# Kernel optimization log

Hardware: AMD Instinct MI355X
Metric: run time of the kernel (lower is better)

Reference implementation:

```python
import math
import jax, jax.numpy as jnp
import numpy as np

B_IN, B_OUT = 16, 16
F_IN, F_OUT, BATCH = 32, 64, 4
N_ALPHA, N_GAMMA = 4, 3
KERNEL_BETA = math.pi / 8.0
L_TOT = sum((2 * l + 1) ** 2 for l in range(B_OUT))  # 5456


def _lg(n):
    return math.lgamma(n + 1.0)


def _small_d(l, beta):
    """Wigner small-d matrix d^l_{m,n}(beta), [2l+1, 2l+1], Condon-Shortley phase."""
    c, s = math.cos(0.5 * beta), math.sin(0.5 * beta)
    d = np.zeros((2 * l + 1, 2 * l + 1), dtype=np.float64)
    for mi, m in enumerate(range(-l, l + 1)):
        for ni, n in enumerate(range(-l, l + 1)):
            pref = 0.5 * (_lg(l + m) + _lg(l - m) + _lg(l + n) + _lg(l - n))
            acc = 0.0
            for k in range(max(0, n - m), min(l + n, l - m) + 1):
                ln = pref - _lg(l + n - k) - _lg(k) - _lg(m - n + k) - _lg(l - m - k)
                acc += ((-1.0) ** (m - n + k)) * math.exp(ln) * (c ** (2 * l + n - m - 2 * k)) * (s ** (m - n + 2 * k))
            d[mi, ni] = acc
    return d


def _qweights(b):
    """Kostelec-Rockmore SOFT quadrature weights over the 2b beta samples."""
    k = np.arange(b)
    w = np.array([
        (2.0 / b) * math.sin(math.pi * (2 * j + 1) / (4.0 * b)) *
        np.sum(np.sin((2 * j + 1) * (2 * k + 1) * math.pi / (4.0 * b)) / (2 * k + 1))
        for j in range(2 * b)])
    return w


def _wigner_table(betas, b_out, scale_fn):
    rows = []
    for beta in betas:
        blocks = [(_small_d(l, beta) * scale_fn(l)).ravel() for l in range(b_out)]
        rows.append(np.concatenate(blocks))
    return np.stack(rows)  # [len(betas), L_TOT]


def _grid_basis(grid, b_out):
    """conj(D^l_{mn}(a,b,g)) = e^{+i m a} d^l_{mn}(b) e^{+i n g}, flattened over (l,m,n)."""
    cols = []
    for (a, bb, g) in grid:
        blocks = []
        for l in range(b_out):
            m = np.arange(-l, l + 1)
            d = _small_d(l, bb)
            ph = np.exp(1j * (m[:, None] * a + m[None, :] * g))
            blocks.append((d * ph).ravel())
        cols.append(np.concatenate(blocks))
    return np.stack(cols, axis=1)  # [L_TOT, n_grid] complex


def _freq_indices(b_out, nfft):
    ms, ns = [], []
    for l in range(b_out):
        r = np.arange(-l, l + 1)
        M, N = np.meshgrid(r, r, indexing='ij')
        ms.append(np.mod(M.ravel(), nfft))
        ns.append(np.mod(N.ravel(), nfft))
    return np.concatenate(ms), np.concatenate(ns)


def make_grid():
    alphas = [2.0 * math.pi * i / N_ALPHA for i in range(N_ALPHA)]
    gammas = [2.0 * math.pi * i / N_GAMMA for i in range(N_GAMMA)]
    return [(a, KERNEL_BETA, g) for a in alphas for g in gammas]


def setup_inputs() -> dict:
    key = jax.random.key(0)
    k1, k2 = jax.random.split(key)
    x = jax.random.normal(k1, (BATCH, F_IN, 2 * B_IN, 2 * B_IN, 2 * B_IN), jnp.float32)
    grid = make_grid()
    n_grid = len(grid)
    stdv = 1.0 / math.sqrt(n_grid * F_IN * (B_OUT ** 3) / float(B_IN ** 3))
    kernel = stdv * jax.random.normal(k2, (F_IN, F_OUT, n_grid), jnp.float32)
    bias = jnp.zeros((1, F_OUT, 1, 1, 1), jnp.float32)
    # analysis table: quadrature weight * d, with (2pi/2b)^2/(8pi^2) = 1/(8 b^2) absorbed
    betas_in = np.pi * (2 * np.arange(2 * B_IN) + 1) / (4.0 * B_IN)
    w = _qweights(B_IN) / (8.0 * B_IN ** 2)
    wig_f = _wigner_table(betas_in, B_OUT, lambda l: 1.0) * w[:, None]
    # synthesis table: (2l+1) * d, times (2b)^2 to cancel ifft2 normalization
    betas_out = np.pi * (2 * np.arange(2 * B_OUT) + 1) / (4.0 * B_OUT)
    wig_i = _wigner_table(betas_out, B_OUT, lambda l: (2 * l + 1) * (2 * B_OUT) ** 2)
    D = _grid_basis(grid, B_OUT)
    return {
        'x': x, 'kernel': kernel, 'bias': bias,
        'wigner_fwd': jnp.asarray(wig_f, jnp.float32),
        'wigner_inv': jnp.asarray(wig_i, jnp.float32),
        'D_re': jnp.asarray(D.real, jnp.float32),
        'D_im': jnp.asarray(D.imag, jnp.float32),
    }


def reference(x, kernel, bias, wigner_fwd, wigner_inv, D_re, D_im):
    batch, fin = x.shape[0], x.shape[1]
    fout = kernel.shape[1]
    midx_in, nidx_in = _freq_indices(B_OUT, 2 * B_IN)
    midx_out, nidx_out = _freq_indices(B_OUT, 2 * B_OUT)
    # --- SO3 FFT of input: FFT over (alpha, gamma), weighted beta-sum with Wigner-d ---
    Xf = jnp.fft.fft2(x.astype(jnp.complex64), axes=(-2, -1))   # [z,i,beta,ma,ng]
    Xg = Xf[..., midx_in, nidx_in]                               # [z,i,beta,L]
    xh = jnp.einsum('bl,zibl->lzi', wigner_fwd.astype(jnp.complex64), Xg)  # [L,z,i]
    # --- local FT of kernel on SO(3) grid points ---
    Dc = jax.lax.complex(D_re, D_im)                             # [L, n_grid]
    yh = jnp.einsum('lj,ioj->lio', Dc, kernel.astype(jnp.complex64))       # [L,i,o]
    # --- per-frequency block matmul (SO3_mm): z^l = x^l @ y^l, contracting f_in ---
    zs, begin = [], 0
    for l in range(B_OUT):
        n = 2 * l + 1
        xl = xh[begin:begin + n * n].reshape(n, n, batch, fin)
        yl = yh[begin:begin + n * n].reshape(n, n, fin, fout)
        zs.append(jnp.einsum('mkzi,knio->mnzo', xl, yl).reshape(n * n, batch, fout))
        begin += n * n
    zh = jnp.concatenate(zs, axis=0)                             # [L,z,o]
    # --- inverse SO3 FFT: scatter (l,m,n) -> FFT bins, ifft over (alpha,gamma) ---
    term = jnp.einsum('bl,lzo->zobl', wigner_inv.astype(jnp.complex64), zh)
    ng = 2 * B_OUT
    Zf = jnp.zeros((batch, fout, ng, ng, ng), jnp.complex64)
    Zf = Zf.at[..., midx_out, nidx_out].add(term)
    out = jnp.fft.ifft2(Zf, axes=(-2, -1)).real.astype(x.dtype)
    return out + bias
```

## Files before the change

### kernel.cpp

```cpp
#include <hip/hip_runtime.h>
#include <math.h>


typedef unsigned short u16;
typedef unsigned int   u32;
typedef __attribute__((ext_vector_type(8))) short  short8;
typedef __attribute__((ext_vector_type(4))) float  floatx4;

constexpr int LTOT = 5456;

constexpr int LB[17] = {0,1,10,35,84,165,286,455,680,969,
                        1330,1771,2300,2925,3654,4495,5456};

__device__ inline u16 f2bf(float f) {
    u32 u = __float_as_uint(f);
    u += 0x7fff + ((u >> 16) & 1);
    return (u16)(u >> 16);
}
__device__ inline u32 pack2bf(float re, float im) {
    return (u32)f2bf(re) | ((u32)f2bf(im) << 16);
}

__global__ __launch_bounds__(256) void k_wtr(const float* __restrict__ w,
                                             float* __restrict__ wT) {
    int t  = blockIdx.x * 256 + threadIdx.x;
    int bq = blockIdx.y;
    if (t < LTOT) {
        float4 v;
        v.x = w[(size_t)(bq * 4 + 0) * LTOT + t];
        v.y = w[(size_t)(bq * 4 + 1) * LTOT + t];
        v.z = w[(size_t)(bq * 4 + 2) * LTOT + t];
        v.w = w[(size_t)(bq * 4 + 3) * LTOT + t];
        *(float4*)(wT + ((size_t)bq * LTOT + t) * 4) = v;
    }
}

__global__ __launch_bounds__(512) void k_fft_fwd(const float* __restrict__ x,
                                                 u32* __restrict__ Xfb) {
    __shared__ float xs[1056];
    __shared__ float Gre[1056], Gim[1056];
    __shared__ float Wc[32], Ws[32];
    int tid = threadIdx.x;
    if (tid < 32) {
        float sv, cv;
        sincosf(6.28318530717958647692f * (float)tid / 32.0f, &sv, &cv);
        Wc[tid] = cv; Ws[tid] = sv;
    }
    const float* src = x + (size_t)blockIdx.x * 1024;
    for (int e = tid; e < 1024; e += 512) xs[(e >> 5) * 33 + (e & 31)] = src[e];
    __syncthreads();
    {
        int a = tid >> 4, k = tid & 15;
        const float* row = &xs[a * 33];
        float Er = 0.f, Ei = 0.f, Or = 0.f, Oi = 0.f;
#pragma unroll
        for (int h = 0; h < 16; h++) {
            int idx = (2 * h * k) & 31;
            float c = Wc[idx], s = Ws[idx];
            float xe = row[2 * h], xo = row[2 * h + 1];
            Er += xe * c;  Ei -= xe * s;
            Or += xo * c;  Oi -= xo * s;
        }
        float WOr = Or * Wc[k] + Oi * Ws[k];
        float WOi = Oi * Wc[k] - Or * Ws[k];
        Gre[a * 33 + k]      = Er + WOr;
        Gim[a * 33 + k]      = Ei + WOi;
        Gre[a * 33 + k + 16] = Er - WOr;
        Gim[a * 33 + k + 16] = Ei - WOi;
    }
    __syncthreads();
    {
        u32* dst = Xfb + (size_t)blockIdx.x * 512;
        int ng = tid & 31, ma = tid >> 5;
        float Er = 0.f, Ei = 0.f, Or = 0.f, Oi = 0.f;
#pragma unroll
        for (int h = 0; h < 16; h++) {
            int idx = (2 * h * ma) & 31;
            float c = Wc[idx], s = Ws[idx];
            float er = Gre[(2 * h) * 33 + ng],      ei = Gim[(2 * h) * 33 + ng];
            float orr = Gre[(2 * h + 1) * 33 + ng], oi = Gim[(2 * h + 1) * 33 + ng];
            Er += er * c + ei * s;   Ei += ei * c - er * s;
            Or += orr * c + oi * s;  Oi += oi * c - orr * s;
        }
        float WOr = Or * Wc[ma] + Oi * Ws[ma];
        float WOi = Oi * Wc[ma] - Or * Ws[ma];
        dst[ma * 32 + ng] = pack2bf(Er + WOr, Ei + WOi);
    }
}

__global__ __launch_bounds__(256) void k_prep_B(const float* __restrict__ Dre,
                                                const float* __restrict__ Dim,
                                                const float* __restrict__ ker,
                                                u32* __restrict__ yhb) {
    __shared__ float Ds[8][24];
    int t0  = blockIdx.x * 8;
    int tid = threadIdx.x;
    if (tid < 192) {
        int rr = tid / 24, jj = tid - rr * 24;
        Ds[rr][jj] = (jj < 12) ? Dre[(t0 + rr) * 12 + jj] : Dim[(t0 + rr) * 12 + jj - 12];
    }
    __syncthreads();
    for (int rep = 0; rep < 8; rep++) {
        int io = rep * 256 + tid;
        const float4* kp = (const float4*)(ker + io * 12);
        float4 ka = kp[0], kb = kp[1], kc = kp[2];
        float kv[12] = {ka.x, ka.y, ka.z, ka.w, kb.x, kb.y, kb.z, kb.w,
                        kc.x, kc.y, kc.z, kc.w};
#pragma unroll
        for (int rr = 0; rr < 8; rr++) {
            float sr = 0.f, si = 0.f;
#pragma unroll
            for (int j = 0; j < 12; j++) {
                sr += Ds[rr][j]      * kv[j];
                si += Ds[rr][12 + j] * kv[j];
            }
            yhb[(size_t)(t0 + rr) * 2048 + io] = pack2bf(sr, si);
        }
    }
}

__global__ __launch_bounds__(256) void k_beta_A(const u32* __restrict__ Xfb,
                                                const float* __restrict__ wfT,
                                                u16* __restrict__ Ab) {
    int ma  = blockIdx.x >> 6;
    int zig = blockIdx.x & 63;
    int tid = threadIdx.x;
    int ng  = tid & 31;
    int lq  = (tid >> 5) & 3;
    int zil = tid >> 7;
    int zi  = zig * 2 + zil;
    int z = zi >> 5, i = zi & 31;
    int mh = (ma <= 15) ? ma : ma - 32;
    int nh = (ng <= 15) ? ng : ng - 32;
    int am = mh < 0 ? -mh : mh;
    int an = nh < 0 ? -nh : nh;
    int l0 = am > an ? am : an;
    int lb = lq * 4;

    int isconj = (ma > 16);
    int mau = isconj ? (32 - ma) : ma;
    int ngu = isconj ? ((32 - ng) & 31) : ng;
    if (mau > 15) { mau = 0; ngu = 0; }

    int tl[4];
#pragma unroll
    for (int j = 0; j < 4; j++) {
        int l = lb + j;
        tl[j] = LB[l] + (mh + l) * (2 * l + 1) + (nh + l);
    }
    float2 acc[4];
#pragma unroll
    for (int j = 0; j < 4; j++) acc[j] = make_float2(0.f, 0.f);

    const u32* xp = Xfb + (size_t)zi * 32 * 512 + mau * 32 + ngu;
    float sgn = isconj ? -1.f : 1.f;
#pragma unroll 2
    for (int bq = 0; bq < 8; bq++) {
        u32 p0 = xp[(size_t)(4 * bq + 0) * 512];
        u32 p1 = xp[(size_t)(4 * bq + 1) * 512];
        u32 p2 = xp[(size_t)(4 * bq + 2) * 512];
        u32 p3 = xp[(size_t)(4 * bq + 3) * 512];
        float vx0 = __uint_as_float(p0 << 16);
        float vy0 = sgn * __uint_as_float(p0 & 0xffff0000u);
        float vx1 = __uint_as_float(p1 << 16);
        float vy1 = sgn * __uint_as_float(p1 & 0xffff0000u);
        float vx2 = __uint_as_float(p2 << 16);
        float vy2 = sgn * __uint_as_float(p2 & 0xffff0000u);
        float vx3 = __uint_as_float(p3 << 16);
        float vy3 = sgn * __uint_as_float(p3 & 0xffff0000u);
        const float4* wq = (const float4*)(wfT + (size_t)bq * (LTOT * 4));
#pragma unroll
        for (int j = 0; j < 4; j++) {
            if (lb + j >= l0) {
                float4 w = wq[tl[j]];
                acc[j].x += w.x * vx0 + w.y * vx1 + w.z * vx2 + w.w * vx3;
                acc[j].y += w.x * vy0 + w.y * vy1 + w.z * vy2 + w.w * vy3;
            }
        }
    }
    int s_i  = i >> 4;
    int kl   = 2 * (i & 15);
    int joff = kl & 7;
    int Lhi  = (kl >> 3) << 4;
#pragma unroll
    for (int j = 0; j < 4; j++) {
        int l = lb + j;
        if (l >= l0) {
            int mi = mh + l, ni = nh + l;
            int s   = 2 * ni + s_i;
            int row = 4 * mi + z;
            u32 pack = pack2bf(acc[j].x, acc[j].y);
            size_t off = (size_t)8192 * l * l + (size_t)s * 4096
                       + ((row >> 4) << 9) + ((Lhi + (row & 15)) << 3) + joff;
            *(u32*)(Ab + off) = pack;
        }
    }
}

__global__ __launch_bounds__(256) void k_gemm(const u16* __restrict__ Ab,
                                              const u32* __restrict__ yhb,
                                              float* __restrict__ zhT) {
    __shared__ __align__(16) u16 As[4096];
    __shared__ __align__(16) u16 Bs[2048];

    int rem = blockIdx.x, l, nl = 1;
    for (l = 15; l >= 0; l--) {
        nl = 2 * l + 1;
        int c = nl * 2;
        if (rem < c) break;
        rem -= c;
    }
    int n  = rem >> 1;
    int oh = rem & 1;
    int base = LB[l];
    const u16* Ag = Ab + (size_t)8192 * l * l;
    int S = 2 * nl;

    int tid = threadIdx.x, lane = tid & 63, w = tid >> 6;

    int kh = (tid >> 4) & 3;
    int nu = ((tid >> 6) << 4) + (tid & 15);
    int oo = (oh << 5) + (nu >> 1);
    int cc = nu & 1;

    floatx4 acc[2][4];
#pragma unroll
    for (int a = 0; a < 2; a++)
#pragma unroll
        for (int b = 0; b < 4; b++) acc[a][b] = (floatx4)0.f;

    for (int s = 0; s < S; s++) {
        const uint4* ap = (const uint4*)(Ag + (size_t)s * 4096);
        uint4 a0 = ap[tid * 2], a1 = ap[tid * 2 + 1];
        int k = s >> 1, ih = s & 1;
        const u32* yr = yhb + (size_t)(base + k * nl + n) * 2048
                        + (((ih << 4) + (kh << 2)) << 6) + oo;
        u32 b0 = yr[0], b1 = yr[64], b2 = yr[128], b3 = yr[192];
        u32 p0, p1, p2, p3;
        if (cc == 0) {
            p0 = (b0 & 0xffffu) | ((b0 >> 16) << 16 ^ 0x80000000u);
            p1 = (b1 & 0xffffu) | ((b1 >> 16) << 16 ^ 0x80000000u);
            p2 = (b2 & 0xffffu) | ((b2 >> 16) << 16 ^ 0x80000000u);
            p3 = (b3 & 0xffffu) | ((b3 >> 16) << 16 ^ 0x80000000u);
        } else {
            p0 = (b0 >> 16) | (b0 << 16);
            p1 = (b1 >> 16) | (b1 << 16);
            p2 = (b2 >> 16) | (b2 << 16);
            p3 = (b3 >> 16) | (b3 << 16);
        }
        {
            uint4* aq = (uint4*)&As[tid << 4];
            aq[0] = a0; aq[1] = a1;
            *(uint4*)&Bs[tid << 3] = make_uint4(p0, p1, p2, p3);
        }
        __syncthreads();
        short8 af0 = *(const short8*)&As[((w << 1) + 0) * 512 + (lane << 3)];
        short8 af1 = *(const short8*)&As[((w << 1) + 1) * 512 + (lane << 3)];
#pragma unroll
        for (int nt = 0; nt < 4; nt++) {
            short8 bf = *(const short8*)&Bs[nt * 512 + (lane << 3)];
            acc[0][nt] = __builtin_amdgcn_mfma_f32_16x16x32_bf16(af0, bf, acc[0][nt], 0, 0, 0);
            acc[1][nt] = __builtin_amdgcn_mfma_f32_16x16x32_bf16(af1, bf, acc[1][nt], 0, 0, 0);
        }
        __syncthreads();
    }

    int q = lane >> 4, cn = lane & 15;
#pragma unroll
    for (int mt = 0; mt < 2; mt++) {
#pragma unroll
        for (int nt = 0; nt < 4; nt++) {
            int nu2 = (nt << 4) + cn;
            int o2  = (oh << 5) + (nu2 >> 1);
            int c2  = nu2 & 1;
#pragma unroll
            for (int r = 0; r < 4; r++) {
                int R = (w << 5) + (mt << 4) + (q << 2) + r;
                int m = R >> 2, z = R & 3;
                if (m < nl) {
                    int t  = base + m * nl + n;
                    int zo = (z << 6) + o2;
                    zhT[((size_t)zo * LTOT + t) * 2 + c2] = acc[mt][nt][r];
                }
            }
        }
    }
}

__global__ __launch_bounds__(256, 8) void k_inv2(const float2* __restrict__ zhT,
                                                 const float* __restrict__ wiT,
                                                 const float* __restrict__ bias,
                                                 float* __restrict__ out) {
    __shared__ float2 Pb[4 * 528];
    __shared__ float Wc[32], Ws[32];
    int tid = threadIdx.x;
    int zo = blockIdx.x & 255;
    int bq = blockIdx.x >> 8;
    int b0 = bq * 4;
    if (tid < 32) {
        float sv, cv;
        sincosf(6.28318530717958647692f * (float)tid / 32.0f, &sv, &cv);
        Wc[tid] = cv; Ws[tid] = sv;
    }
    {
        int ng = tid & 31, rq = tid >> 5;
        int nh = (ng <= 15) ? ng : ng - 32;
        int an = nh < 0 ? -nh : nh;
        const float2* zr = zhT + (size_t)zo * LTOT;
        const float4* wp = (const float4*)(wiT + (size_t)bq * (LTOT * 4));
#pragma unroll
        for (int mr = 0; mr < 2; mr++) {
            int ma = rq + 8 * mr;
            int l0 = ma > an ? ma : an;
            float2 a0 = make_float2(0.f, 0.f), a1 = a0, a2 = a0, a3 = a0;
#pragma unroll 4
            for (int l = 0; l < 16; l++) {
                if (l >= l0) {
                    int t = LB[l] + (ma + l) * (2 * l + 1) + (nh + l);
                    float2 zv = zr[t];
                    float4 w = wp[t];
                    a0.x += w.x * zv.x; a0.y += w.x * zv.y;
                    a1.x += w.y * zv.x; a1.y += w.y * zv.y;
                    a2.x += w.z * zv.x; a2.y += w.z * zv.y;
                    a3.x += w.w * zv.x; a3.y += w.w * zv.y;
                }
            }
            int po = ma * 33 + ng;
            Pb[po]            = a0;
            Pb[528 + po]      = a1;
            Pb[2 * 528 + po]  = a2;
            Pb[3 * 528 + po]  = a3;
        }
    }
    __syncthreads();
#pragma unroll
    for (int it = 0; it < 2; it++) {
        int task = tid + it * 256;
        int rowid = task >> 3, q = task & 7;
        float2* prow = &Pb[(rowid >> 4) * 528 + (rowid & 15) * 33];
        float2 E0 = make_float2(0.f, 0.f), O0 = E0, E1 = E0, O1 = E0;
        int k1 = q + 8;
#pragma unroll 4
        for (int h = 0; h < 16; h++) {
            float2 e = prow[2 * h], o = prow[2 * h + 1];
            int i0 = (2 * h * q) & 31;
            int i1 = (2 * h * k1) & 31;
            float c0 = Wc[i0], s0 = Ws[i0];
            float c1 = Wc[i1], s1 = Ws[i1];
            E0.x += e.x * c0 - e.y * s0;  E0.y += e.x * s0 + e.y * c0;
            O0.x += o.x * c0 - o.y * s0;  O0.y += o.x * s0 + o.y * c0;
            E1.x += e.x * c1 - e.y * s1;  E1.y += e.x * s1 + e.y * c1;
            O1.x += o.x * c1 - o.y * s1;  O1.y += o.x * s1 + o.y * c1;
        }
        float c0 = Wc[q],  s0 = Ws[q];
        float c1 = Wc[k1], s1 = Ws[k1];
        float2 w0 = make_float2(O0.x * c0 - O0.y * s0, O0.x * s0 + O0.y * c0);
        float2 w1 = make_float2(O1.x * c1 - O1.y * s1, O1.x * s1 + O1.y * c1);
        prow[q]      = make_float2(E0.x + w0.x, E0.y + w0.y);
        prow[q + 16] = make_float2(E0.x - w0.x, E0.y - w0.y);
        prow[q + 8]  = make_float2(E1.x + w1.x, E1.y + w1.y);
        prow[q + 24] = make_float2(E1.x - w1.x, E1.y - w1.y);
    }
    __syncthreads();
    float bv = bias[zo & 63];
#pragma unroll
    for (int it = 0; it < 2; it++) {
        int task = tid + it * 256;
        int p = task >> 7, rr = task & 127;
        int qa = rr >> 5, g = rr & 31;
        const float2* pc = &Pb[p * 528];
        float2 c0 = pc[g];
        float Ea[4], Oa[4];
#pragma unroll
        for (int jj = 0; jj < 4; jj++) { Ea[jj] = c0.x; Oa[jj] = 0.f; }
#pragma unroll 4
        for (int j = 1; j < 8; j++) {
            float2 c = pc[(2 * j) * 33 + g];
#pragma unroll
            for (int jj = 0; jj < 4; jj++) {
                int a = qa * 4 + jj;
                int idx = ((2 * j) * a) & 31;
                Ea[jj] += 2.f * (c.x * Wc[idx] - c.y * Ws[idx]);
            }
        }
#pragma unroll 4
        for (int j = 0; j < 8; j++) {
            float2 c = pc[(2 * j + 1) * 33 + g];
#pragma unroll
            for (int jj = 0; jj < 4; jj++) {
                int a = qa * 4 + jj;
                int idx = ((2 * j + 1) * a) & 31;
                Oa[jj] += 2.f * (c.x * Wc[idx] - c.y * Ws[idx]);
            }
        }
        float* dst = out + (size_t)zo * 32768 + (size_t)(b0 + p) * 1024;
#pragma unroll
        for (int jj = 0; jj < 4; jj++) {
            int a = qa * 4 + jj;
            dst[a * 32 + g]        = (Ea[jj] + Oa[jj]) * (1.f / 1024.f) + bv;
            dst[(a + 16) * 32 + g] = (Ea[jj] - Oa[jj]) * (1.f / 1024.f) + bv;
        }
    }
}

extern "C" void kernel_launch(void* const* d_in, const int* in_sizes, int n_in,
                              void* d_out, int out_size, void* d_ws, size_t ws_size,
                              hipStream_t stream) {
    const float* x    = (const float*)d_in[0];
    const float* ker  = (const float*)d_in[1];
    const float* bias = (const float*)d_in[2];
    const float* wf   = (const float*)d_in[3];
    const float* wi   = (const float*)d_in[4];
    const float* Dre  = (const float*)d_in[5];
    const float* Dim  = (const float*)d_in[6];
    float* out = (float*)d_out;

    char* ws = (char*)d_ws;
    u32*    yhb = (u32*)ws;
    u16*    Ab  = (u16*)(ws + 44695552);
    float*  zhT = (float*)(ws + 44695552 + 4194304);
    u32*    Xfb = (u32*)zhT;
    float*  wfT = (float*)(ws + 44695552 + 4194304 + 8388608);
    float*  wiT = (float*)ws;

    hipLaunchKernelGGL(k_fft_fwd, dim3(4096),  dim3(512), 0, stream, x, Xfb);
    hipLaunchKernelGGL(k_wtr,     dim3(22, 8), dim3(256), 0, stream, wf, wfT);
    hipLaunchKernelGGL(k_prep_B,  dim3(682),   dim3(256), 0, stream, Dre, Dim, ker, yhb);
    hipLaunchKernelGGL(k_beta_A,  dim3(2048),  dim3(256), 0, stream, Xfb, wfT, Ab);
    hipLaunchKernelGGL(k_gemm,    dim3(512),   dim3(256), 0, stream, Ab, yhb, zhT);
    hipLaunchKernelGGL(k_wtr,     dim3(22, 8), dim3(256), 0, stream, wi, wiT);
    hipLaunchKernelGGL(k_inv2,    dim3(2048),  dim3(256), 0, stream,
                       (const float2*)zhT, wiT, bias, out);
}
```

Baseline: 239.0 us.

## Double-buffer B tile, load A fragments directly to registers, prefetch next step

The per-frequency GEMM kernel no longer stages the A operand through shared memory. Each wave reads its A fragments straight from global memory into registers, and the B tile is double-buffered in LDS so one barrier per k-step suffices instead of two. The global loads for step s+1 are issued before the MFMAs of step s, overlapping memory latency with compute. This costs extra registers for the prefetched values and relies on the A layout already matching the per-lane fragment order.

```diff
diff --git a/kernel.cpp b/kernel.cpp
--- a/kernel.cpp
+++ b/kernel.cpp
@@ -200,8 +200,7 @@
 __global__ __launch_bounds__(256) void k_gemm(const u16* __restrict__ Ab,
                                               const u32* __restrict__ yhb,
                                               float* __restrict__ zhT) {
-    __shared__ __align__(16) u16 As[4096];
-    __shared__ __align__(16) u16 Bs[2048];
+    __shared__ __align__(16) u16 Bs[2][2048];
 
     int rem = blockIdx.x, l, nl = 1;
     for (l = 15; l >= 0; l--) {
@@ -223,20 +222,19 @@
     int oo = (oh << 5) + (nu >> 1);
     int cc = nu & 1;
 
+    const u32* ybase = yhb + (size_t)(base + n) * 2048 + (kh << 8) + oo;
+    const u16* Aw = Ag + ((w << 10) | (lane << 3));
+
     floatx4 acc[2][4];
 #pragma unroll
     for (int a = 0; a < 2; a++)
 #pragma unroll
         for (int b = 0; b < 4; b++) acc[a][b] = (floatx4)0.f;
 
-    for (int s = 0; s < S; s++) {
-        const uint4* ap = (const uint4*)(Ag + (size_t)s * 4096);
-        uint4 a0 = ap[tid * 2], a1 = ap[tid * 2 + 1];
-        int k = s >> 1, ih = s & 1;
-        const u32* yr = yhb + (size_t)(base + k * nl + n) * 2048
-                        + (((ih << 4) + (kh << 2)) << 6) + oo;
-        u32 b0 = yr[0], b1 = yr[64], b2 = yr[128], b3 = yr[192];
-        u32 p0, p1, p2, p3;
+    u32 p0, p1, p2, p3;
+    short8 a0r, a1r;
+    {
+        u32 b0 = ybase[0], b1 = ybase[64], b2 = ybase[128], b3 = ybase[192];
         if (cc == 0) {
             p0 = (b0 & 0xffffu) | ((b0 >> 16) << 16 ^ 0x80000000u);
             p1 = (b1 & 0xffffu) | ((b1 >> 16) << 16 ^ 0x80000000u);
@@ -248,21 +246,40 @@
             p2 = (b2 >> 16) | (b2 << 16);
             p3 = (b3 >> 16) | (b3 << 16);
         }
-        {
-            uint4* aq = (uint4*)&As[tid << 4];
-            aq[0] = a0; aq[1] = a1;
-            *(uint4*)&Bs[tid << 3] = make_uint4(p0, p1, p2, p3);
-        }
+        a0r = *(const short8*)(Aw);
+        a1r = *(const short8*)(Aw + 512);
+    }
+
+    for (int s = 0; s < S; s++) {
+        int cur = s & 1;
+        *(uint4*)&Bs[cur][tid << 3] = make_uint4(p0, p1, p2, p3);
+        short8 af0 = a0r, af1 = a1r;
         __syncthreads();
-        short8 af0 = *(const short8*)&As[((w << 1) + 0) * 512 + (lane << 3)];
-        short8 af1 = *(const short8*)&As[((w << 1) + 1) * 512 + (lane << 3)];
+        if (s + 1 < S) {
+            int sn = s + 1;
+            int k = sn >> 1, ih = sn & 1;
+            const u32* yr = ybase + (size_t)k * nl * 2048 + (ih << 10);
+            u32 b0 = yr[0], b1 = yr[64], b2 = yr[128], b3 = yr[192];
+            if (cc == 0) {
+                p0 = (b0 & 0xffffu) | ((b0 >> 16) << 16 ^ 0x80000000u);
+                p1 = (b1 & 0xffffu) | ((b1 >> 16) << 16 ^ 0x80000000u);
+                p2 = (b2 & 0xffffu) | ((b2 >> 16) << 16 ^ 0x80000000u);
+                p3 = (b3 & 0xffffu) | ((b3 >> 16) << 16 ^ 0x80000000u);
+            } else {
+                p0 = (b0 >> 16) | (b0 << 16);
+                p1 = (b1 >> 16) | (b1 << 16);
+                p2 = (b2 >> 16) | (b2 << 16);
+                p3 = (b3 >> 16) | (b3 << 16);
+            }
+            a0r = *(const short8*)(Aw + (size_t)sn * 4096);
+            a1r = *(const short8*)(Aw + (size_t)sn * 4096 + 512);
+        }
 #pragma unroll
         for (int nt = 0; nt < 4; nt++) {
-            short8 bf = *(const short8*)&Bs[nt * 512 + (lane << 3)];
+            short8 bf = *(const short8*)&Bs[cur][nt * 512 + (lane << 3)];
             acc[0][nt] = __builtin_amdgcn_mfma_f32_16x16x32_bf16(af0, bf, acc[0][nt], 0, 0, 0);
             acc[1][nt] = __builtin_amdgcn_mfma_f32_16x16x32_bf16(af1, bf, acc[1][nt], 0, 0, 0);
         }
-        __syncthreads();
     }
 
     int q = lane >> 4, cn = lane & 15;
```

Result: no change. 240.2 us (+0.5%).

## Store kernel FT in MFMA fragment order and load GEMM operands directly to registers

Applied to the files above, without the earlier changes.

The kernel-FT prep now writes yhb in a permuted layout that matches the MFMA B-fragment order, so the GEMM can load each lane's operand with contiguous uint4 loads. The GEMM drops its LDS staging and both __syncthreads per step, reads A and B fragments straight from global memory, and forms the complex-conjugate pair layout with v_perm plus an xor. Loads are double-buffered across even and odd steps so the next fetch overlaps the MFMAs. In exchange it uses more registers and relies on cache hits instead of shared memory for reuse.

```diff
diff --git a/kernel.cpp b/kernel.cpp
--- a/kernel.cpp
+++ b/kernel.cpp
@@ -19,6 +19,15 @@
 }
 __device__ inline u32 pack2bf(float re, float im) {
     return (u32)f2bf(re) | ((u32)f2bf(im) << 16);
+}
+
+__device__ inline short8 btr4(uint4 q, u32 sel, u32 msk) {
+    uint4 t;
+    t.x = __builtin_amdgcn_perm(q.x, q.x, sel) ^ msk;
+    t.y = __builtin_amdgcn_perm(q.y, q.y, sel) ^ msk;
+    t.z = __builtin_amdgcn_perm(q.z, q.z, sel) ^ msk;
+    t.w = __builtin_amdgcn_perm(q.w, q.w, sel) ^ msk;
+    return *(short8*)&t;
 }
 
 __global__ __launch_bounds__(256) void k_wtr(const float* __restrict__ w,
@@ -102,6 +111,9 @@
     __syncthreads();
     for (int rep = 0; rep < 8; rep++) {
         int io = rep * 256 + tid;
+        int i  = io >> 6, o = io & 63;
+        int nio = ((i >> 4) << 10) + ((o >> 5) << 9) + (((o >> 3) & 3) << 7)
+                + (((i >> 2) & 3) << 5) + ((o & 7) << 2) + (i & 3);
         const float4* kp = (const float4*)(ker + io * 12);
         float4 ka = kp[0], kb = kp[1], kc = kp[2];
         float kv[12] = {ka.x, ka.y, ka.z, ka.w, kb.x, kb.y, kb.z, kb.w,
@@ -114,7 +126,7 @@
                 sr += Ds[rr][j]      * kv[j];
                 si += Ds[rr][12 + j] * kv[j];
             }
-            yhb[(size_t)(t0 + rr) * 2048 + io] = pack2bf(sr, si);
+            yhb[(size_t)(t0 + rr) * 2048 + nio] = pack2bf(sr, si);
         }
     }
 }
@@ -200,9 +212,6 @@
 __global__ __launch_bounds__(256) void k_gemm(const u16* __restrict__ Ab,
                                               const u32* __restrict__ yhb,
                                               float* __restrict__ zhT) {
-    __shared__ __align__(16) u16 As[4096];
-    __shared__ __align__(16) u16 Bs[2048];
-
     int rem = blockIdx.x, l, nl = 1;
     for (l = 15; l >= 0; l--) {
         nl = 2 * l + 1;
@@ -217,11 +226,12 @@
     int S = 2 * nl;
 
     int tid = threadIdx.x, lane = tid & 63, w = tid >> 6;
-
-    int kh = (tid >> 4) & 3;
-    int nu = ((tid >> 6) << 4) + (tid & 15);
-    int oo = (oh << 5) + (nu >> 1);
-    int cc = nu & 1;
+    int cc = lane & 1;
+    u32 sel = cc ? 0x01000302u : 0x03020100u;
+    u32 msk = cc ? 0u          : 0x80000000u;
+
+    const u32* Bb = yhb + (size_t)(base + n) * 2048 + (oh << 9) + ((lane >> 1) << 2);
+    const u16* Aw = Ag + ((w << 10) | (lane << 3));
 
     floatx4 acc[2][4];
 #pragma unroll
@@ -229,41 +239,40 @@
 #pragma unroll
         for (int b = 0; b < 4; b++) acc[a][b] = (floatx4)0.f;
 
-    for (int s = 0; s < S; s++) {
-        const uint4* ap = (const uint4*)(Ag + (size_t)s * 4096);
-        uint4 a0 = ap[tid * 2], a1 = ap[tid * 2 + 1];
-        int k = s >> 1, ih = s & 1;
-        const u32* yr = yhb + (size_t)(base + k * nl + n) * 2048
-                        + (((ih << 4) + (kh << 2)) << 6) + oo;
-        u32 b0 = yr[0], b1 = yr[64], b2 = yr[128], b3 = yr[192];
-        u32 p0, p1, p2, p3;
-        if (cc == 0) {
-            p0 = (b0 & 0xffffu) | ((b0 >> 16) << 16 ^ 0x80000000u);
-            p1 = (b1 & 0xffffu) | ((b1 >> 16) << 16 ^ 0x80000000u);
-            p2 = (b2 & 0xffffu) | ((b2 >> 16) << 16 ^ 0x80000000u);
-            p3 = (b3 & 0xffffu) | ((b3 >> 16) << 16 ^ 0x80000000u);
-        } else {
-            p0 = (b0 >> 16) | (b0 << 16);
-            p1 = (b1 >> 16) | (b1 << 16);
-            p2 = (b2 >> 16) | (b2 << 16);
-            p3 = (b3 >> 16) | (b3 << 16);
-        }
-        {
-            uint4* aq = (uint4*)&As[tid << 4];
-            aq[0] = a0; aq[1] = a1;
-            *(uint4*)&Bs[tid << 3] = make_uint4(p0, p1, p2, p3);
-        }
-        __syncthreads();
-        short8 af0 = *(const short8*)&As[((w << 1) + 0) * 512 + (lane << 3)];
-        short8 af1 = *(const short8*)&As[((w << 1) + 1) * 512 + (lane << 3)];
-#pragma unroll
-        for (int nt = 0; nt < 4; nt++) {
-            short8 bf = *(const short8*)&Bs[nt * 512 + (lane << 3)];
-            acc[0][nt] = __builtin_amdgcn_mfma_f32_16x16x32_bf16(af0, bf, acc[0][nt], 0, 0, 0);
-            acc[1][nt] = __builtin_amdgcn_mfma_f32_16x16x32_bf16(af1, bf, acc[1][nt], 0, 0, 0);
-        }
-        __syncthreads();
-    }
+#define LOADB(s, q0, q1, q2, q3) { \
+    const uint4* bp = (const uint4*)(Bb + (size_t)((s) >> 1) * nl * 2048 + (((s) & 1) << 10)); \
+    q0 = bp[0]; q1 = bp[32]; q2 = bp[64]; q3 = bp[96]; }
+#define LOADA(s, r0, r1) { \
+    const u16* apx = Aw + (size_t)(s) * 4096; \
+    r0 = *(const short8*)apx; r1 = *(const short8*)(apx + 512); }
+#define MF(a, b, c) __builtin_amdgcn_mfma_f32_16x16x32_bf16(a, b, c, 0, 0, 0)
+
+    uint4 eB0, eB1, eB2, eB3; short8 ea0, ea1;
+    uint4 oB0, oB1, oB2, oB3; short8 oa0, oa1;
+    LOADA(0, ea0, ea1); LOADB(0, eB0, eB1, eB2, eB3);
+    LOADA(1, oa0, oa1); LOADB(1, oB0, oB1, oB2, oB3);
+
+    for (int s = 0; s < S; s += 2) {
+        short8 bf0 = btr4(eB0, sel, msk), bf1 = btr4(eB1, sel, msk);
+        short8 bf2 = btr4(eB2, sel, msk), bf3 = btr4(eB3, sel, msk);
+        short8 af0 = ea0, af1 = ea1;
+        if (s + 2 < S) { LOADA(s + 2, ea0, ea1); LOADB(s + 2, eB0, eB1, eB2, eB3); }
+        acc[0][0] = MF(af0, bf0, acc[0][0]);  acc[1][0] = MF(af1, bf0, acc[1][0]);
+        acc[0][1] = MF(af0, bf1, acc[0][1]);  acc[1][1] = MF(af1, bf1, acc[1][1]);
+        acc[0][2] = MF(af0, bf2, acc[0][2]);  acc[1][2] = MF(af1, bf2, acc[1][2]);
+        acc[0][3] = MF(af0, bf3, acc[0][3]);  acc[1][3] = MF(af1, bf3, acc[1][3]);
+        short8 cf0 = btr4(oB0, sel, msk), cf1 = btr4(oB1, sel, msk);
+        short8 cf2 = btr4(oB2, sel, msk), cf3 = btr4(oB3, sel, msk);
+        short8 ag0 = oa0, ag1 = oa1;
+        if (s + 3 < S) { LOADA(s + 3, oa0, oa1); LOADB(s + 3, oB0, oB1, oB2, oB3); }
+        acc[0][0] = MF(ag0, cf0, acc[0][0]);  acc[1][0] = MF(ag1, cf0, acc[1][0]);
+        acc[0][1] = MF(ag0, cf1, acc[0][1]);  acc[1][1] = MF(ag1, cf1, acc[1][1]);
+        acc[0][2] = MF(ag0, cf2, acc[0][2]);  acc[1][2] = MF(ag1, cf2, acc[1][2]);
+        acc[0][3] = MF(ag0, cf3, acc[0][3]);  acc[1][3] = MF(ag1, cf3, acc[1][3]);
+    }
+#undef LOADB
+#undef LOADA
+#undef MF
 
     int q = lane >> 4, cn = lane & 15;
 #pragma unroll
```

After: 224.3 us. 1.07x faster.
